# Kernel tuning notes

Hardware: AMD Instinct MI355X
Metric: run time of the kernel (lower is better)

## Reference

```python
import jax, jax.numpy as jnp
import numpy as np

WINDOW_SIZE = 9
EPS = 1e-05


def _box_sum(x, w):
    """Zero-padded 3D box-filter sum, computed separably (one 1D conv per axis).
    Identical math to conv3d with an all-ones [w,w,w] kernel and zero padding."""
    pad = w // 2
    dn = ('NCDHW', 'OIDHW', 'NCDHW')
    for ax in range(3):  # D, H, W
        kshape = [1, 1, 1, 1, 1]
        kshape[2 + ax] = w
        kernel = jnp.ones(kshape, x.dtype)
        padding = [(0, 0)] * 3
        padding[ax] = (pad, pad)
        x = jax.lax.conv_general_dilated(x, kernel, (1, 1, 1), padding,
                                         dimension_numbers=dn)
    return x


def setup_inputs() -> dict:
    key = jax.random.key(0)
    k1, k2 = jax.random.split(key)
    shape = (2, 1, 160, 160, 160)
    predicted = jax.random.uniform(k1, shape, dtype=jnp.float32)
    target = jax.random.uniform(k2, shape, dtype=jnp.float32)
    return {"predicted": predicted, "target": target}


def reference(predicted, target):
    I = predicted.astype(jnp.float32)
    J = target.astype(jnp.float32)
    w = WINDOW_SIZE
    win_size = jnp.float32(w ** 3)

    I_sum = _box_sum(I, w)
    J_sum = _box_sum(J, w)
    I2_sum = _box_sum(I * I, w)
    J2_sum = _box_sum(J * J, w)
    IJ_sum = _box_sum(I * J, w)

    u_I = I_sum / win_size
    u_J = J_sum / win_size

    cross = IJ_sum - u_J * I_sum - u_I * J_sum + u_I * u_J * win_size
    I_var = I2_sum - 2.0 * u_I * I_sum + u_I * u_I * win_size
    J_var = J2_sum - 2.0 * u_J * J_sum + u_J * u_J * win_size

    cc = cross * cross / (I_var * J_var + EPS)
    cc = jnp.clip(cc, 0.0, 1.0)
    return 1.0 - jnp.mean(cc)
```

## Files before the change

kernel.cpp:

```cpp
#include <hip/hip_runtime.h>
#include <hip/hip_fp16.h>


#define DIM 160
#define HW  (160 * 160)
#define VOL (160 * 160 * 160)
#define NBATCH 2
#define TH 8
#define SR 16
#define THB 320
#define SEG 10
#define NSEG (DIM / SEG)

struct __align__(16) h8 { __half2 a, b, c, d; };
struct __align__(8) h4 { __half2 a, b; };
typedef float v2f __attribute__((ext_vector_type(2)));

__device__ inline float4 dec8(unsigned int u) {
    v2f lo = __builtin_amdgcn_cvt_pk_f32_fp8((int)u, false);
    v2f hi = __builtin_amdgcn_cvt_pk_f32_fp8((int)u, true);
    return make_float4(lo[0], lo[1], hi[0], hi[1]);
}

__device__ inline unsigned int enc8(float a, float b, float c, float d) {
    int u = __builtin_amdgcn_cvt_pk_fp8_f32(a, b, 0, false);
    u = __builtin_amdgcn_cvt_pk_fp8_f32(c, d, u, true);
    return (unsigned int)u;
}

__global__ __launch_bounds__(THB) void k1_boxsum2d(const float* __restrict__ I,
                                                   const float* __restrict__ J,
                                                   unsigned char* __restrict__ A8) {
    __shared__ __half wsl[5][SR][DIM];

    const int tid = threadIdx.x;
    const int orig = blockIdx.x;
    const int wgid = (orig & 7) * 400 + (orig >> 3);
    const int ty = wgid % 20;
    const int rest = wgid / 20;
    const int dz = rest % 80;
    const int batch = rest / 80;
    const int h0 = ty * TH;
    const int d0 = 2 * dz;
    const float* Ib = I + (size_t)batch * VOL;
    const float* Jb = J + (size_t)batch * VOL;

    const int r = tid / 20, g = tid % 20;
    const int gh = h0 - 4 + r;
    const int gw = 8 * g - 4;
    const bool rowok = (gh >= 0) && (gh < DIM);

    float a[16], b[16], a2[16], b2[16];

#define LOADROW(d, A_, B_)                                                  \
    if (rowok) {                                                            \
        const float* pI = Ib + (size_t)(d) * HW + gh * DIM;                 \
        const float* pJ = Jb + (size_t)(d) * HW + gh * DIM;                 \
        _Pragma("unroll")                                                   \
        for (int q = 0; q < 4; ++q) {                                       \
            int c0 = gw + 4 * q;    \
            if (c0 >= 0 && c0 < DIM) {                                      \
                *(float4*)&A_[4 * q] = *(const float4*)(pI + c0);           \
                *(float4*)&B_[4 * q] = *(const float4*)(pJ + c0);           \
            } else {                                                        \
                *(float4*)&A_[4 * q] = make_float4(0.f, 0.f, 0.f, 0.f);     \
                *(float4*)&B_[4 * q] = make_float4(0.f, 0.f, 0.f, 0.f);     \
            }                                                               \
        }                                                                   \
    }

#define WSTAGE(A_, B_)                                                      \
    {                                                                       \
        __half* wrow = &wsl[0][0][0] + (r * DIM + 8 * g);                   \
        if (!rowok) {                                                       \
            const __half2 hz = __float2half2_rn(0.f);                       \
            h8 z; z.a = hz; z.b = hz; z.c = hz; z.d = hz;                   \
            _Pragma("unroll")                                               \
            for (int ch = 0; ch < 5; ++ch)                                  \
                *(h8*)(wrow + ch * (SR * DIM)) = z;                         \
        } else {                                                            \
            PROC(0, A_[k], wrow)                                            \
            PROC(1, B_[k], wrow)                                            \
            PROC(2, A_[k] * A_[k], wrow)                                    \
            PROC(3, B_[k] * B_[k], wrow)                                    \
            PROC(4, A_[k] * B_[k], wrow)                                    \
        }                                                                   \
    }

#define PROC(CH, VAL, WROW)                                                 \
    {                                                                       \
        float o[8];                                                         \
        float ss = 0.f;                                                     \
        _Pragma("unroll")                                                   \
        for (int k = 0; k < 9; ++k) { ss += (VAL); }                        \
        o[0] = ss;                                                          \
        _Pragma("unroll")                                                   \
        for (int j = 1; j < 8; ++j) {                                       \
            int k = j + 8; float add_ = (VAL);                              \
            k = j - 1;     float sub_ = (VAL);                              \
            ss += add_ - sub_;                                              \
            o[j] = ss;                                                      \
        }                                                                   \
        h8 v;                                                               \
        v.a = __floats2half2_rn(o[0], o[1]);                                \
        v.b = __floats2half2_rn(o[2], o[3]);                                \
        v.c = __floats2half2_rn(o[4], o[5]);                                \
        v.d = __floats2half2_rn(o[6], o[7]);                                \
        *(h8*)(WROW + CH * (SR * DIM)) = v;                                 \
    }

#define HSTAGE(d)                                                           \
    {                                                                       \
        const int q = tid % 40, r8 = tid / 40;                              \
        const int wp0 = 2 * q;                                              \
        const size_t ob = (size_t)batch * 5 * VOL + (size_t)(d) * HW +      \
                          (size_t)(h0 + r8) * DIM + 4 * q;                  \
        _Pragma("unroll")                                                   \
        for (int ch = 0; ch < 5; ++ch) {                                    \
            const __half2* col = (const __half2*)&wsl[ch][r8][0] + wp0;     \
            h4 v = *(const h4*)col;                                         \
            __half2 sa = v.a, sb = v.b;                                     \
            _Pragma("unroll")                                               \
            for (int k = 1; k < 9; ++k) {                                   \
                h4 u = *(const h4*)(col + k * (DIM / 2));                   \
                sa = __hadd2(sa, u.a);                                      \
                sb = __hadd2(sb, u.b);                                      \
            }                                                               \
            float2 f0 = __half22float2(sa);                                 \
            float2 f1 = __half22float2(sb);                                 \
            *(unsigned int*)(A8 + ob + (size_t)ch * VOL) =                  \
                enc8(f0.x, f0.y, f1.x, f1.y);                               \
        }                                                                   \
    }

    LOADROW(d0, a, b)
    WSTAGE(a, b)
    __syncthreads();
    LOADROW(d0 + 1, a2, b2)
    HSTAGE(d0)
    __syncthreads();
    WSTAGE(a2, b2)
    __syncthreads();
    HSTAGE(d0 + 1)

#undef LOADROW
#undef WSTAGE
#undef PROC
#undef HSTAGE
}

__device__ inline void cc_accum(float s0, float s1, float s2, float s3,
                                float s4, float& acc) {
    const float inv_wsz = 1.0f / 729.0f;
    float cross = s4 - s0 * s1 * inv_wsz;
    float Ivar  = s2 - s0 * s0 * inv_wsz;
    float Jvar  = s3 - s1 * s1 * inv_wsz;
    float cc = cross * cross * __builtin_amdgcn_rcpf(Ivar * Jvar + 1e-5f);
    acc += fminf(fmaxf(cc, 0.0f), 1.0f);
}

__global__ __launch_bounds__(256) void k2_dsum_final(const unsigned char* __restrict__ A8,
                                                     float* __restrict__ partial) {
    const int batch = blockIdx.y;
    const unsigned int* B = (const unsigned int*)(A8 + (size_t)batch * 5 * VOL);
    const int PLW = VOL / 4;
    const int HWW = HW / 4;
    int t = blockIdx.x * 256 + threadIdx.x;
    int wq = t % 40;
    int rest = t / 40;
    int h = rest % DIM;
    int seg = rest / DIM;
    int d0 = seg * SEG;
    const int base = h * 40 + wq;

    float4 s0 = {0,0,0,0}, s1 = {0,0,0,0}, s2 = {0,0,0,0},
           s3 = {0,0,0,0}, s4 = {0,0,0,0};
#define ACC4(sv, ch, idx, sgn)                                              \
    {                                                                       \
        float4 v_ = dec8(B[(ch) * PLW + (idx)]);                            \
        sv.x sgn v_.x; sv.y sgn v_.y; sv.z sgn v_.z; sv.w sgn v_.w;         \
    }
#pragma unroll
    for (int k = -4; k <= 4; ++k) {
        int dd = d0 + k;
        if (dd >= 0) {
            int idx = base + dd * HWW;
            ACC4(s0, 0, idx, +=) ACC4(s1, 1, idx, +=) ACC4(s2, 2, idx, +=)
            ACC4(s3, 3, idx, +=) ACC4(s4, 4, idx, +=)
        }
    }

    float acc = 0.f;
    for (int d = d0; d < d0 + SEG; ++d) {
        cc_accum(s0.x, s1.x, s2.x, s3.x, s4.x, acc);
        cc_accum(s0.y, s1.y, s2.y, s3.y, s4.y, acc);
        cc_accum(s0.z, s1.z, s2.z, s3.z, s4.z, acc);
        cc_accum(s0.w, s1.w, s2.w, s3.w, s4.w, acc);
        int lead = d + 5, trail = d - 4;
        if (lead < DIM) {
            int li = base + lead * HWW;
            ACC4(s0, 0, li, +=) ACC4(s1, 1, li, +=) ACC4(s2, 2, li, +=)
            ACC4(s3, 3, li, +=) ACC4(s4, 4, li, +=)
        }
        if (trail >= 0) {
            int ti = base + trail * HWW;
            ACC4(s0, 0, ti, -=) ACC4(s1, 1, ti, -=) ACC4(s2, 2, ti, -=)
            ACC4(s3, 3, ti, -=) ACC4(s4, 4, ti, -=)
        }
    }
#undef ACC4

#pragma unroll
    for (int off = 32; off > 0; off >>= 1) acc += __shfl_down(acc, off);
    __shared__ float ws4[4];
    if ((threadIdx.x & 63) == 0) ws4[threadIdx.x >> 6] = acc;
    __syncthreads();
    if (threadIdx.x == 0)
        partial[batch * 400 + blockIdx.x] = ws4[0] + ws4[1] + ws4[2] + ws4[3];
}

__global__ __launch_bounds__(256) void final_reduce(const float* __restrict__ partial,
                                                    int n, float* __restrict__ out) {
    float a = 0.f;
    for (int i = threadIdx.x; i < n; i += 256) a += partial[i];
#pragma unroll
    for (int off = 32; off > 0; off >>= 1) a += __shfl_down(a, off);
    __shared__ float ws4[4];
    if ((threadIdx.x & 63) == 0) ws4[threadIdx.x >> 6] = a;
    __syncthreads();
    if (threadIdx.x == 0)
        out[0] = 1.0f - (ws4[0] + ws4[1] + ws4[2] + ws4[3]) *
                            (1.0f / (float)(NBATCH * VOL));
}

extern "C" void kernel_launch(void* const* d_in, const int* in_sizes, int n_in,
                              void* d_out, int out_size, void* d_ws, size_t ws_size,
                              hipStream_t stream) {
    const float* I = (const float*)d_in[0];
    const float* J = (const float*)d_in[1];
    float* out = (float*)d_out;

    unsigned char* A8 = (unsigned char*)d_ws;
    float* partial = (float*)(A8 + (size_t)NBATCH * 5 * VOL);

    k1_boxsum2d<<<20 * 80 * NBATCH, THB, 0, stream>>>(I, J, A8);
    dim3 g2(400, NBATCH);
    k2_dsum_final<<<g2, 256, 0, stream>>>(A8, partial);
    final_reduce<<<1, 256, 0, stream>>>(partial, NBATCH * 400, out);
}
```

Measured before the change: 55.60 us.

## Process 8 depth slices per block with double-buffered LDS and packed fp16 sums

Each k1 block now handles a chunk of 8 consecutive depth slices instead of 2. It double-buffers shared-memory staging and prefetches the next slice's rows while the current slice's H-direction sums run. The W-direction sums for I, J, I² and J² are computed in packed half2 arithmetic (I and J packed together), with only the I·J product kept in fp32, which roughly halves ALU work. The cost is fewer blocks, so less parallelism, plus extra fp16 rounding error in the squared-term sums. It also sets a launch-bounds occupancy hint.

```diff
diff --git a/kernel.cpp b/kernel.cpp
--- a/kernel.cpp
+++ b/kernel.cpp
@@ -9,12 +9,14 @@
 #define TH 8
 #define SR 16
 #define THB 320
+#define DCHUNK 8
 #define SEG 10
 #define NSEG (DIM / SEG)
 
-struct __align__(16) h8 { __half2 a, b, c, d; };
-struct __align__(8) h4 { __half2 a, b; };
+typedef __fp16 hh2 __attribute__((ext_vector_type(2)));
 typedef float v2f __attribute__((ext_vector_type(2)));
+struct __align__(16) h8f { hh2 a, b, c, d; };
+struct __align__(8)  h4f { hh2 a, b; };
 
 __device__ inline float4 dec8(unsigned int u) {
     v2f lo = __builtin_amdgcn_cvt_pk_f32_fp8((int)u, false);
@@ -28,20 +30,22 @@
     return (unsigned int)u;
 }
 
-__global__ __launch_bounds__(THB) void k1_boxsum2d(const float* __restrict__ I,
-                                                   const float* __restrict__ J,
-                                                   unsigned char* __restrict__ A8) {
-    __shared__ __half wsl[5][SR][DIM];
+__global__ __launch_bounds__(THB, 3) void k1_boxsum2d(const float* __restrict__ I,
+                                                      const float* __restrict__ J,
+                                                      unsigned char* __restrict__ A8) {
+    __shared__ hh2    wAB[2][SR][DIM];
+    __shared__ hh2    wQQ[2][SR][DIM];
+    __shared__ __fp16 wIJ[2][SR][DIM];
 
     const int tid = threadIdx.x;
     const int orig = blockIdx.x;
-    const int wgid = (orig & 7) * 400 + (orig >> 3);
+    const int wgid = (orig & 7) * 100 + (orig >> 3);
     const int ty = wgid % 20;
     const int rest = wgid / 20;
-    const int dz = rest % 80;
-    const int batch = rest / 80;
+    const int c8 = rest % 20;
+    const int batch = rest / 20;
     const int h0 = ty * TH;
-    const int d0 = 2 * dz;
+    const int d0 = c8 * DCHUNK;
     const float* Ib = I + (size_t)batch * VOL;
     const float* Jb = J + (size_t)batch * VOL;
 
@@ -49,103 +53,138 @@
     const int gh = h0 - 4 + r;
     const int gw = 8 * g - 4;
     const bool rowok = (gh >= 0) && (gh < DIM);
-
-    float a[16], b[16], a2[16], b2[16];
-
-#define LOADROW(d, A_, B_)                                                  \
+    const int q = tid % 40, r8 = tid / 40;
+
+    float a[2][16], b[2][16];
+
+#define LOADROW(d, s)                                                       \
     if (rowok) {                                                            \
         const float* pI = Ib + (size_t)(d) * HW + gh * DIM;                 \
         const float* pJ = Jb + (size_t)(d) * HW + gh * DIM;                 \
         _Pragma("unroll")                                                   \
-        for (int q = 0; q < 4; ++q) {                                       \
-            int c0 = gw + 4 * q;    \
+        for (int qq = 0; qq < 4; ++qq) {                                    \
+            int c0 = gw + 4 * qq;   \
             if (c0 >= 0 && c0 < DIM) {                                      \
-                *(float4*)&A_[4 * q] = *(const float4*)(pI + c0);           \
-                *(float4*)&B_[4 * q] = *(const float4*)(pJ + c0);           \
+                *(float4*)&a[s][4 * qq] = *(const float4*)(pI + c0);        \
+                *(float4*)&b[s][4 * qq] = *(const float4*)(pJ + c0);        \
             } else {                                                        \
-                *(float4*)&A_[4 * q] = make_float4(0.f, 0.f, 0.f, 0.f);     \
-                *(float4*)&B_[4 * q] = make_float4(0.f, 0.f, 0.f, 0.f);     \
+                *(float4*)&a[s][4 * qq] = make_float4(0.f, 0.f, 0.f, 0.f);  \
+                *(float4*)&b[s][4 * qq] = make_float4(0.f, 0.f, 0.f, 0.f);  \
             }                                                               \
         }                                                                   \
     }
 
-#define WSTAGE(A_, B_)                                                      \
+#define WSTAGE(s, bf)                                                       \
     {                                                                       \
-        __half* wrow = &wsl[0][0][0] + (r * DIM + 8 * g);                   \
         if (!rowok) {                                                       \
-            const __half2 hz = __float2half2_rn(0.f);                       \
-            h8 z; z.a = hz; z.b = hz; z.c = hz; z.d = hz;                   \
+            h8f z; z.a = (hh2)0; z.b = (hh2)0; z.c = (hh2)0; z.d = (hh2)0;  \
+            *(h8f*)&wAB[bf][r][8 * g] = z;                                  \
+            *(h8f*)&wAB[bf][r][8 * g + 4] = z;                              \
+            *(h8f*)&wQQ[bf][r][8 * g] = z;                                  \
+            *(h8f*)&wQQ[bf][r][8 * g + 4] = z;                              \
+            *(h8f*)&wIJ[bf][r][8 * g] = z;                                  \
+        } else {                                                            \
+            hh2 hab[16], hsq[16];                                           \
             _Pragma("unroll")                                               \
-            for (int ch = 0; ch < 5; ++ch)                                  \
-                *(h8*)(wrow + ch * (SR * DIM)) = z;                         \
-        } else {                                                            \
-            PROC(0, A_[k], wrow)                                            \
-            PROC(1, B_[k], wrow)                                            \
-            PROC(2, A_[k] * A_[k], wrow)                                    \
-            PROC(3, B_[k] * B_[k], wrow)                                    \
-            PROC(4, A_[k] * B_[k], wrow)                                    \
+            for (int k = 0; k < 16; ++k) {                                  \
+                hab[k] = __builtin_amdgcn_cvt_pkrtz(a[s][k], b[s][k]);      \
+                hsq[k] = hab[k] * hab[k];                                   \
+            }                                                               \
+            hh2 oA[8], oQ[8];                                               \
+            {                                                               \
+                hh2 sA = hab[0], sQ = hsq[0];                               \
+                _Pragma("unroll")                                           \
+                for (int k = 1; k < 9; ++k) { sA += hab[k]; sQ += hsq[k]; } \
+                oA[0] = sA; oQ[0] = sQ;                                     \
+                _Pragma("unroll")                                           \
+                for (int j = 1; j < 8; ++j) {                               \
+                    sA += hab[j + 8] - hab[j - 1];                          \
+                    sQ += hsq[j + 8] - hsq[j - 1];                          \
+                    oA[j] = sA; oQ[j] = sQ;                                 \
+                }                                                           \
+            }                                                               \
+            float pij[16];                                                  \
+            _Pragma("unroll")                                               \
+            for (int k = 0; k < 16; ++k) pij[k] = a[s][k] * b[s][k];        \
+            float oI[8];                                                    \
+            {                                                               \
+                float ss = pij[0];                                          \
+                _Pragma("unroll")                                           \
+                for (int k = 1; k < 9; ++k) ss += pij[k];                   \
+                oI[0] = ss;                                                 \
+                _Pragma("unroll")                                           \
+                for (int j = 1; j < 8; ++j) {                               \
+                    ss += pij[j + 8] - pij[j - 1];                          \
+                    oI[j] = ss;                                             \
+                }                                                           \
+            }                                                               \
+            h8f vA, vQ, vI;                                                 \
+            vA.a = oA[0]; vA.b = oA[1]; vA.c = oA[2]; vA.d = oA[3];         \
+            *(h8f*)&wAB[bf][r][8 * g] = vA;                                 \
+            vA.a = oA[4]; vA.b = oA[5]; vA.c = oA[6]; vA.d = oA[7];         \
+            *(h8f*)&wAB[bf][r][8 * g + 4] = vA;                             \
+            vQ.a = oQ[0]; vQ.b = oQ[1]; vQ.c = oQ[2]; vQ.d = oQ[3];         \
+            *(h8f*)&wQQ[bf][r][8 * g] = vQ;                                 \
+            vQ.a = oQ[4]; vQ.b = oQ[5]; vQ.c = oQ[6]; vQ.d = oQ[7];         \
+            *(h8f*)&wQQ[bf][r][8 * g + 4] = vQ;                             \
+            vI.a = __builtin_amdgcn_cvt_pkrtz(oI[0], oI[1]);                \
+            vI.b = __builtin_amdgcn_cvt_pkrtz(oI[2], oI[3]);                \
+            vI.c = __builtin_amdgcn_cvt_pkrtz(oI[4], oI[5]);                \
+            vI.d = __builtin_amdgcn_cvt_pkrtz(oI[6], oI[7]);                \
+            *(h8f*)&wIJ[bf][r][8 * g] = vI;                                 \
         }                                                                   \
     }
 
-#define PROC(CH, VAL, WROW)                                                 \
+#define HSTAGE(bf, dsl)                                                     \
     {                                                                       \
-        float o[8];                                                         \
-        float ss = 0.f;                                                     \
+        const hh2* pA = &wAB[bf][r8][4 * q];                                \
+        const hh2* pQ = &wQQ[bf][r8][4 * q];                                \
+        const __fp16* pI = &wIJ[bf][r8][4 * q];                             \
+        h8f vA = *(const h8f*)pA;                                           \
+        hh2 aA0 = vA.a, aA1 = vA.b, aA2 = vA.c, aA3 = vA.d;                 \
+        h8f vQ = *(const h8f*)pQ;                                           \
+        hh2 aQ0 = vQ.a, aQ1 = vQ.b, aQ2 = vQ.c, aQ3 = vQ.d;                 \
+        h4f vI = *(const h4f*)pI;                                           \
+        hh2 aI0 = vI.a, aI1 = vI.b;                                         \
         _Pragma("unroll")                                                   \
-        for (int k = 0; k < 9; ++k) { ss += (VAL); }                        \
-        o[0] = ss;                                                          \
-        _Pragma("unroll")                                                   \
-        for (int j = 1; j < 8; ++j) {                                       \
-            int k = j + 8; float add_ = (VAL);                              \
-            k = j - 1;     float sub_ = (VAL);                              \
-            ss += add_ - sub_;                                              \
-            o[j] = ss;                                                      \
+        for (int k = 1; k < 9; ++k) {                                       \
+            vA = *(const h8f*)(pA + k * DIM);                               \
+            aA0 += vA.a; aA1 += vA.b; aA2 += vA.c; aA3 += vA.d;             \
+            vQ = *(const h8f*)(pQ + k * DIM);                               \
+            aQ0 += vQ.a; aQ1 += vQ.b; aQ2 += vQ.c; aQ3 += vQ.d;             \
+            vI = *(const h4f*)(pI + k * DIM);                               \
+            aI0 += vI.a; aI1 += vI.b;                                       \
         }                                                                   \
-        h8 v;                                                               \
-        v.a = __floats2half2_rn(o[0], o[1]);                                \
-        v.b = __floats2half2_rn(o[2], o[3]);                                \
-        v.c = __floats2half2_rn(o[4], o[5]);                                \
-        v.d = __floats2half2_rn(o[6], o[7]);                                \
-        *(h8*)(WROW + CH * (SR * DIM)) = v;                                 \
-    }
-
-#define HSTAGE(d)                                                           \
-    {                                                                       \
-        const int q = tid % 40, r8 = tid / 40;                              \
-        const int wp0 = 2 * q;                                              \
-        const size_t ob = (size_t)batch * 5 * VOL + (size_t)(d) * HW +      \
+        const size_t ob = (size_t)batch * 5 * VOL + (size_t)(dsl) * HW +    \
                           (size_t)(h0 + r8) * DIM + 4 * q;                  \
-        _Pragma("unroll")                                                   \
-        for (int ch = 0; ch < 5; ++ch) {                                    \
-            const __half2* col = (const __half2*)&wsl[ch][r8][0] + wp0;     \
-            h4 v = *(const h4*)col;                                         \
-            __half2 sa = v.a, sb = v.b;                                     \
-            _Pragma("unroll")                                               \
-            for (int k = 1; k < 9; ++k) {                                   \
-                h4 u = *(const h4*)(col + k * (DIM / 2));                   \
-                sa = __hadd2(sa, u.a);                                      \
-                sb = __hadd2(sb, u.b);                                      \
-            }                                                               \
-            float2 f0 = __half22float2(sa);                                 \
-            float2 f1 = __half22float2(sb);                                 \
-            *(unsigned int*)(A8 + ob + (size_t)ch * VOL) =                  \
-                enc8(f0.x, f0.y, f1.x, f1.y);                               \
-        }                                                                   \
-    }
-
-    LOADROW(d0, a, b)
-    WSTAGE(a, b)
+        *(unsigned int*)(A8 + ob + 0 * (size_t)VOL) =                       \
+            enc8((float)aA0[0], (float)aA1[0], (float)aA2[0], (float)aA3[0]); \
+        *(unsigned int*)(A8 + ob + 1 * (size_t)VOL) =                       \
+            enc8((float)aA0[1], (float)aA1[1], (float)aA2[1], (float)aA3[1]); \
+        *(unsigned int*)(A8 + ob + 2 * (size_t)VOL) =                       \
+            enc8((float)aQ0[0], (float)aQ1[0], (float)aQ2[0], (float)aQ3[0]); \
+        *(unsigned int*)(A8 + ob + 3 * (size_t)VOL) =                       \
+            enc8((float)aQ0[1], (float)aQ1[1], (float)aQ2[1], (float)aQ3[1]); \
+        *(unsigned int*)(A8 + ob + 4 * (size_t)VOL) =                       \
+            enc8((float)aI0[0], (float)aI0[1], (float)aI1[0], (float)aI1[1]); \
+    }
+
+    LOADROW(d0, 0)
+    LOADROW(d0 + 1, 1)
+    WSTAGE(0, 0)
     __syncthreads();
-    LOADROW(d0 + 1, a2, b2)
-    HSTAGE(d0)
-    __syncthreads();
-    WSTAGE(a2, b2)
-    __syncthreads();
-    HSTAGE(d0 + 1)
+#pragma unroll
+    for (int i = 0; i < DCHUNK; ++i) {
+        if (i + 2 < DCHUNK) LOADROW(d0 + i + 2, i & 1)
+        HSTAGE(i & 1, d0 + i)
+        if (i + 1 < DCHUNK) {
+            WSTAGE((i + 1) & 1, (i + 1) & 1)
+            __syncthreads();
+        }
+    }
 
 #undef LOADROW
 #undef WSTAGE
-#undef PROC
 #undef HSTAGE
 }
 
@@ -243,7 +282,7 @@
     unsigned char* A8 = (unsigned char*)d_ws;
     float* partial = (float*)(A8 + (size_t)NBATCH * 5 * VOL);
 
-    k1_boxsum2d<<<20 * 80 * NBATCH, THB, 0, stream>>>(I, J, A8);
+    k1_boxsum2d<<<20 * (DIM / DCHUNK) * NBATCH, THB, 0, stream>>>(I, J, A8);
     dim3 g2(400, NBATCH);
     k2_dsum_final<<<g2, 256, 0, stream>>>(A8, partial);
     final_reduce<<<1, 256, 0, stream>>>(partial, NBATCH * 400, out);
```

Measured after the change: 80.21 us. +44.3%, slower.
